# Kernel optimization log

Hardware: AMD Instinct MI355X
Metric: run time of the kernel (lower is better)

## Reference

```python
import jax, jax.numpy as jnp
import numpy as np

SLOPE = 0.01   # LeakyReLU default negative slope
EPS = 1e-5     # InstanceNorm eps
PAD = 6        # shift-search border

def _pad(x):
    # ReplicationPad (1,1) on H and W (depth pad is 0, depth==1 anyway)
    return jnp.pad(x, ((0, 0), (0, 0), (1, 1), (1, 1)), mode='edge')

def _conv(x, w, b):
    y = jax.lax.conv_general_dilated(x, w, (1, 1), 'VALID',
                                     dimension_numbers=('NCHW', 'OIHW', 'NCHW'))
    return y + b[None, :, None, None]

def _inorm(x):
    # InstanceNorm3d (affine=False) over (D,H,W); D==1 so over (H,W) per (b,c)
    m = jnp.mean(x, axis=(-2, -1), keepdims=True)
    v = jnp.mean((x - m) ** 2, axis=(-2, -1), keepdims=True)
    return (x - m) * jax.lax.rsqrt(v + EPS)

def _lrelu(x):
    return jnp.where(x >= 0, x, SLOPE * x)

def setup_inputs() -> dict:
    key = jax.random.key(0)
    ks = jax.random.split(key, 8)
    B, H, W = 8, 256, 256
    xIn = jax.random.normal(ks[0], (B, 1, H, W), jnp.float32)
    target = jax.random.normal(ks[1], (B, 1, H, W), jnp.float32)
    w0 = jax.random.normal(ks[2], (64, 1, 3, 3), jnp.float32) * 0.1
    b0 = jax.random.normal(ks[3], (64,), jnp.float32) * 0.1
    ws = jax.random.normal(ks[4], (7, 64, 64, 3, 3), jnp.float32) * 0.05
    bs = jax.random.normal(ks[5], (7, 64), jnp.float32) * 0.05
    wp = jax.random.normal(ks[6], (1, 64, 3, 3), jnp.float32) * 0.05
    bp = jax.random.normal(ks[7], (1,), jnp.float32) * 0.05
    return {'xIn': xIn, 'target': target, 'w0': w0, 'b0': b0,
            'ws': ws, 'bs': bs, 'wp': wp, 'bp': bp}

def reference(xIn, target, w0, b0, ws, bs, wp, bp):
    x = _lrelu(_inorm(_conv(_pad(xIn), w0, b0)))
    for i in range(7):
        x = _lrelu(_inorm(_conv(_pad(x), ws[i], bs[i])))
    # projection + residual
    hr = _conv(_pad(x), wp, bp) + xIn  # (B,1,H,W)

    # vectorized findBestLoss: 13x13 shift search
    B, C, H, W = hr.shape
    h, w = H - 2 * PAD, W - 2 * PAD
    t = hr.dtype.type(0) + target[..., PAD:H - PAD, PAD:W - PAD]  # (B,C,h,w)
    offs = jnp.stack(jnp.meshgrid(jnp.arange(13), jnp.arange(13),
                                  indexing='ij'), -1).reshape(-1, 2)  # (169,2)

    def _slice(off):
        return jax.lax.dynamic_slice(hr, (0, 0, off[0], off[1]), (B, C, h, w))

    crops = jax.vmap(_slice)(offs)  # (169,B,C,h,w)
    eq = jax.lax.stop_gradient(
        jnp.mean(t[None] - crops, axis=(2, 3, 4), keepdims=True))  # detached equalizer
    losses = jnp.mean((crops + eq - t[None]) ** 2, axis=(2, 3, 4))  # (169,B)
    loss = jnp.mean(jnp.min(losses, axis=0))
    return hr, loss
```

## Files before the change

### kernel.cpp

```cpp
#include <hip/hip_runtime.h>

#define B_ 8
#define C_ 64
#define HW_ 65536
#define SLOPE_ 0.01f
#define EPS_ 1e-5f
#define CROP_ 244
#define NPIX_ 59536.0f

typedef unsigned short u16;
typedef __attribute__((ext_vector_type(8))) _Float16 f16x8;
typedef __attribute__((ext_vector_type(2))) _Float16 f16x2;
typedef __attribute__((ext_vector_type(4))) float f32x4;

__device__ __forceinline__ int clampi(int v, int lo, int hi) { return v < lo ? lo : (v > hi ? hi : v); }

__device__ __forceinline__ u16 f2h(float f) {
    union { _Float16 h; u16 u; } v; v.h = (_Float16)f; return v.u;
}
__device__ __forceinline__ float h2f(u16 b) {
    union { u16 u; _Float16 h; } v; v.u = b; return (float)v.h;
}
__device__ __forceinline__ f16x2 lrelu2(f16x2 a) {
    const f16x2 z = {(_Float16)0.f, (_Float16)0.f};
    const f16x2 sl = {(_Float16)SLOPE_, (_Float16)SLOPE_};
    return __builtin_elementwise_max(a, z) + sl * __builtin_elementwise_min(a, z);
}

__global__ void wtrans_kernel(const float* __restrict__ ws, u16* __restrict__ wH) {
    int idx = blockIdx.x * 256 + threadIdx.x;
    if (idx >= 7 * 36864) return;
    int l = idx / 36864;
    int rem = idx - l * 36864;
    int frag = rem >> 9;
    int lj = rem & 511;
    int lane = lj >> 3, j = lj & 7;
    int tap = frag >> 3, kb = (frag >> 2) & 1, mt = frag & 3;
    int oc = (mt << 4) + (lane & 15);
    int ic = (kb << 5) + ((lane >> 4) << 3) + j;
    wH[idx] = f2h(ws[((l * 64 + oc) * 64 + ic) * 9 + tap]);
}

__global__ __launch_bounds__(256) void conv0_kernel(
    const float* __restrict__ xin, const float* __restrict__ w0,
    const float* __restrict__ b0, u16* __restrict__ yout) {
    __shared__ float w0s[576];
    __shared__ float b0s[64];
    int tid = threadIdx.x;
    for (int i = tid; i < 576; i += 256) w0s[i] = w0[i];
    if (tid < 64) b0s[tid] = b0[tid];
    __syncthreads();
    int b = blockIdx.x & 7;
    int px = (blockIdx.x >> 3) * 256 + tid;
    int pxg = (b << 16) + px;
    int y = px >> 8, x = px & 255;
    float xv[9];
#pragma unroll
    for (int ky = 0; ky < 3; ky++)
#pragma unroll
        for (int kx = 0; kx < 3; kx++)
            xv[ky * 3 + kx] = xin[(b << 16) + (clampi(y + ky - 1, 0, 255) << 8) + clampi(x + kx - 1, 0, 255)];
    float acc[64];
#pragma unroll
    for (int k = 0; k < 64; k++) acc[k] = b0s[k];
#pragma unroll
    for (int t = 0; t < 9; t++) {
        float v = xv[t];
#pragma unroll
        for (int k = 0; k < 64; k++) acc[k] = fmaf(v, w0s[k * 9 + t], acc[k]);
    }
    uint4* op = (uint4*)(yout + ((size_t)pxg << 6));
#pragma unroll
    for (int c8 = 0; c8 < 8; c8++) {
        uint4 o;
        o.x = (unsigned)f2h(acc[c8 * 8 + 0]) | ((unsigned)f2h(acc[c8 * 8 + 1]) << 16);
        o.y = (unsigned)f2h(acc[c8 * 8 + 2]) | ((unsigned)f2h(acc[c8 * 8 + 3]) << 16);
        o.z = (unsigned)f2h(acc[c8 * 8 + 4]) | ((unsigned)f2h(acc[c8 * 8 + 5]) << 16);
        o.w = (unsigned)f2h(acc[c8 * 8 + 6]) | ((unsigned)f2h(acc[c8 * 8 + 7]) << 16);
        op[c8] = o;
    }
}

__global__ __launch_bounds__(256) void stats0_kernel(const u16* __restrict__ yin, float* __restrict__ partial) {
    __shared__ float red[4][64][2];
    int tid = threadIdx.x;
    int b = blockIdx.x & 7, tile = blockIdx.x >> 3;
    int pxl = tid >> 3, c8 = tid & 7;
    float s[8], s2[8];
#pragma unroll
    for (int i = 0; i < 8; i++) { s[i] = 0.f; s2[i] = 0.f; }
    for (int it = 0; it < 8; it++) {
        int px = (tile << 8) + (it << 5) + pxl;
        f16x8 v = *(const f16x8*)(yin + ((((size_t)(b << 16)) + px) << 6) + (c8 << 3));
#pragma unroll
        for (int i = 0; i < 8; i++) {
            float f = (float)v[i];
            s[i] += f; s2[i] += f * f;
        }
    }
#pragma unroll
    for (int msk = 8; msk <= 32; msk <<= 1)
#pragma unroll
        for (int i = 0; i < 8; i++) {
            s[i] += __shfl_xor(s[i], msk);
            s2[i] += __shfl_xor(s2[i], msk);
        }
    int lane = tid & 63, wv = tid >> 6;
    if (lane < 8) {
#pragma unroll
        for (int i = 0; i < 8; i++) {
            red[wv][lane * 8 + i][0] = s[i];
            red[wv][lane * 8 + i][1] = s2[i];
        }
    }
    __syncthreads();
    if (tid < 128) {
        int oc = tid >> 1, k2 = tid & 1;
        float v = red[0][oc][k2] + red[1][oc][k2] + red[2][oc][k2] + red[3][oc][k2];
        partial[(((b << 8) + tile) << 7) + (oc << 1) + k2] = v;
    }
}

__global__ __launch_bounds__(64) void statfin_kernel(const float* __restrict__ partial, float* __restrict__ normp) {
    int b = blockIdx.x >> 6, oc = blockIdx.x & 63;
    int lane = threadIdx.x;
    float s = 0.f, s2 = 0.f;
#pragma unroll
    for (int i = 0; i < 4; i++) {
        int t = lane + (i << 6);
        const float* p = partial + (((b << 8) + t) << 7) + (oc << 1);
        s += p[0]; s2 += p[1];
    }
#pragma unroll
    for (int msk = 1; msk < 64; msk <<= 1) { s += __shfl_xor(s, msk); s2 += __shfl_xor(s2, msk); }
    if (lane == 0) {
        float mean = s * (1.0f / HW_);
        float var = s2 * (1.0f / HW_) - mean * mean;
        float inv = rsqrtf(var + EPS_);
        normp[blockIdx.x * 2] = inv;
        normp[blockIdx.x * 2 + 1] = -mean * inv;
    }
}

__global__ __launch_bounds__(256, 3) void conv_mid_kernel(
    const u16* __restrict__ yin, const float* __restrict__ normp,
    const u16* __restrict__ wH, const float* __restrict__ bias,
    u16* __restrict__ yout, float* __restrict__ partial) {
    __shared__ u16 s_in[324 * 64];
    __shared__ unsigned s_invk[32];
    __shared__ unsigned s_betak[32];
    __shared__ float s_bias[64];
    __shared__ float s_red[4][64][2];

    int tid = threadIdx.x;
    int b = blockIdx.x & 7;
    int tile = blockIdx.x >> 3;
    int ty = tile >> 4, tx = tile & 15;
    int y0 = ty << 4, x0 = tx << 4;

    if (tid < 64) s_bias[tid] = bias[tid];
    if (tid < 32) {
        float4 ld = ((const float4*)(normp + (b << 7)))[tid];
        union { unsigned u; f16x2 h; } iv, bv;
        iv.h = (f16x2){(_Float16)ld.x, (_Float16)ld.z};
        bv.h = (f16x2){(_Float16)ld.y, (_Float16)ld.w};
        s_invk[tid] = iv.u;
        s_betak[tid] = bv.u;
    }
    __syncthreads();

    for (int chunk = tid; chunk < 2592; chunk += 256) {
        int px = chunk >> 3, c8 = chunk & 7;
        int row = px / 18;
        int col = px - row * 18;
        int iy = clampi(y0 - 1 + row, 0, 255);
        int ix = clampi(x0 - 1 + col, 0, 255);
        union { uint4 q; f16x2 h2[4]; } ui, uo;
        ui.q = *(const uint4*)(yin + ((((size_t)(b << 16)) + (iy << 8) + ix) << 6) + (c8 << 3));
#pragma unroll
        for (int p = 0; p < 4; p++) {
            union { unsigned u; f16x2 h; } iv, bv;
            iv.u = s_invk[(c8 << 2) + p];
            bv.u = s_betak[(c8 << 2) + p];
            f16x2 a = ui.h2[p] * iv.h + bv.h;
            uo.h2[p] = lrelu2(a);
        }
        int phys = c8 ^ (px & 7);
        *(uint4*)(&s_in[(px << 6) + (phys << 3)]) = uo.q;
    }
    __syncthreads();

    int lane = tid & 63, wv = tid >> 6;
    int m = lane & 15, q = lane >> 4;
    int r0 = wv << 2;

    f32x4 acc[4][4];
#pragma unroll
    for (int a = 0; a < 4; a++)
#pragma unroll
        for (int c = 0; c < 4; c++) acc[a][c] = (f32x4){0.f, 0.f, 0.f, 0.f};

    const f16x8* wfp = (const f16x8*)wH;
    f16x8 wcur[8], wnxt[8];
#pragma unroll
    for (int f = 0; f < 8; f++) wcur[f] = wfp[(f << 6) + lane];

#pragma unroll 1
    for (int t = 0; t < 9; t++) {
        if (t < 8) {
            const f16x8* wn = wfp + ((t + 1) << 9);
#pragma unroll
            for (int f = 0; f < 8; f++) wnxt[f] = wn[(f << 6) + lane];
        }
        int ky = t / 3, kx = t - ky * 3;
#pragma unroll
        for (int nt = 0; nt < 4; nt++) {
            int row = r0 + nt + ky;
            int p = row * 18 + kx + m;
            int key = p & 7;
            const u16* pin = &s_in[p << 6];
            f16x8 bf0 = *(const f16x8*)(pin + ((q ^ key) << 3));
            f16x8 bf1 = *(const f16x8*)(pin + (((4 + q) ^ key) << 3));
#pragma unroll
            for (int mt = 0; mt < 4; mt++)
                acc[mt][nt] = __builtin_amdgcn_mfma_f32_16x16x32_f16(wcur[mt], bf0, acc[mt][nt], 0, 0, 0);
#pragma unroll
            for (int mt = 0; mt < 4; mt++)
                acc[mt][nt] = __builtin_amdgcn_mfma_f32_16x16x32_f16(wcur[4 + mt], bf1, acc[mt][nt], 0, 0, 0);
        }
        if (t < 8) {
#pragma unroll
            for (int f = 0; f < 8; f++) wcur[f] = wnxt[f];
        }
    }

    float ss[4][4], sq[4][4];
#pragma unroll
    for (int mt = 0; mt < 4; mt++)
#pragma unroll
        for (int r = 0; r < 4; r++) { ss[mt][r] = 0.f; sq[mt][r] = 0.f; }

#pragma unroll
    for (int mt = 0; mt < 4; mt++) {
        int ocb = (mt << 4) + (q << 2);
        float b0v = s_bias[ocb], b1v = s_bias[ocb + 1], b2v = s_bias[ocb + 2], b3v = s_bias[ocb + 3];
#pragma unroll
        for (int nt = 0; nt < 4; nt++) {
            f32x4 v = acc[mt][nt];
            float v0 = v.x + b0v, v1 = v.y + b1v, v2 = v.z + b2v, v3 = v.w + b3v;
            uint2 o;
            o.x = (unsigned)f2h(v0) | ((unsigned)f2h(v1) << 16);
            o.y = (unsigned)f2h(v2) | ((unsigned)f2h(v3) << 16);
            int y = y0 + r0 + nt, x = x0 + m;
            *(uint2*)(yout + ((((size_t)(b << 16)) + (y << 8) + x) << 6) + ocb) = o;
            ss[mt][0] += v0; ss[mt][1] += v1; ss[mt][2] += v2; ss[mt][3] += v3;
            sq[mt][0] += v0 * v0; sq[mt][1] += v1 * v1; sq[mt][2] += v2 * v2; sq[mt][3] += v3 * v3;
        }
    }
#pragma unroll
    for (int mt = 0; mt < 4; mt++)
#pragma unroll
        for (int r = 0; r < 4; r++) {
#pragma unroll
            for (int msk = 1; msk <= 8; msk <<= 1) {
                ss[mt][r] += __shfl_xor(ss[mt][r], msk);
                sq[mt][r] += __shfl_xor(sq[mt][r], msk);
            }
        }
    if (m == 0) {
#pragma unroll
        for (int mt = 0; mt < 4; mt++)
#pragma unroll
            for (int r = 0; r < 4; r++) {
                int oc = (mt << 4) + (q << 2) + r;
                s_red[wv][oc][0] = ss[mt][r];
                s_red[wv][oc][1] = sq[mt][r];
            }
    }
    __syncthreads();
    if (tid < 128) {
        int oc = tid >> 1, k2 = tid & 1;
        float v = s_red[0][oc][k2] + s_red[1][oc][k2] + s_red[2][oc][k2] + s_red[3][oc][k2];
        partial[(((b << 8) + tile) << 7) + (oc << 1) + k2] = v;
    }
}

__global__ __launch_bounds__(256) void proj_kernel(
    const u16* __restrict__ y7, const float* __restrict__ normp,
    const float* __restrict__ wp, const float* __restrict__ bp,
    const float* __restrict__ xin, float* __restrict__ out) {
    __shared__ u16 s_a[18 * 66 * 8];
    __shared__ unsigned s_invk[32];
    __shared__ unsigned s_betak[32];
    __shared__ unsigned s_w2[288];

    int tid = threadIdx.x;
    int b = blockIdx.x & 7, slab = blockIdx.x >> 3;
    int sy = slab >> 2, sx = slab & 3;
    int y0 = sy << 4, x0 = sx << 6;

    if (tid < 32) {
        float4 ld = ((const float4*)(normp + (b << 7)))[tid];
        union { unsigned u; f16x2 h; } iv, bv;
        iv.h = (f16x2){(_Float16)ld.x, (_Float16)ld.z};
        bv.h = (f16x2){(_Float16)ld.y, (_Float16)ld.w};
        s_invk[tid] = iv.u;
        s_betak[tid] = bv.u;
    }
    for (int i = tid; i < 288; i += 256) {
        int pr = i / 9, tap = i - pr * 9;
        int ch = pr << 1;
        s_w2[i] = (unsigned)f2h(wp[ch * 9 + tap]) | ((unsigned)f2h(wp[(ch + 1) * 9 + tap]) << 16);
    }
    __syncthreads();

    int col = tid & 63, prow = tid >> 6;
    float acc[4];
#pragma unroll
    for (int r = 0; r < 4; r++) acc[r] = bp[0];

    for (int c8 = 0; c8 < 8; c8++) {
        for (int idx = tid; idx < 1188; idx += 256) {
            int row = idx / 66;
            int cc = idx - row * 66;
            int iy = clampi(y0 - 1 + row, 0, 255);
            int ix = clampi(x0 - 1 + cc, 0, 255);
            union { uint4 q; f16x2 h2[4]; } ui, uo;
            ui.q = *(const uint4*)(y7 + ((((size_t)(b << 16)) + (iy << 8) + ix) << 6) + (c8 << 3));
#pragma unroll
            for (int p = 0; p < 4; p++) {
                union { unsigned u; f16x2 h; } iv, bv;
                iv.u = s_invk[(c8 << 2) + p];
                bv.u = s_betak[(c8 << 2) + p];
                uo.h2[p] = lrelu2(ui.h2[p] * iv.h + bv.h);
            }
            *(uint4*)(&s_a[idx << 3]) = uo.q;
        }
        __syncthreads();

#pragma unroll
        for (int ky = 0; ky < 3; ky++)
#pragma unroll
            for (int kx = 0; kx < 3; kx++) {
                int tap = ky * 3 + kx;
                float w[8];
#pragma unroll
                for (int p = 0; p < 4; p++) {
                    unsigned wu = s_w2[((c8 << 2) + p) * 9 + tap];
                    w[2 * p] = h2f((u16)(wu & 0xffff));
                    w[2 * p + 1] = h2f((u16)(wu >> 16));
                }
#pragma unroll
                for (int rr = 0; rr < 4; rr++) {
                    int lrow = prow * 4 + rr + ky;
                    f16x8 v = *(const f16x8*)(&s_a[(lrow * 66 + col + kx) << 3]);
#pragma unroll
                    for (int i = 0; i < 8; i++)
                        acc[rr] = fmaf((float)v[i], w[i], acc[rr]);
                }
            }
        __syncthreads();
    }

#pragma unroll
    for (int rr = 0; rr < 4; rr++) {
        int pxg = (b << 16) + ((y0 + prow * 4 + rr) << 8) + x0 + col;
        out[pxg] = acc[rr] + xin[pxg];
    }
}

__global__ __launch_bounds__(256) void loss_main_kernel(
    const float* __restrict__ hr, const float* __restrict__ target,
    float* __restrict__ lossS) {
    int b = blockIdx.x & 7, off = blockIdx.x >> 3;
    int oy = off / 13, ox = off - oy * 13;
    const float* hp = hr + b * HW_ + (oy << 8) + ox;
    const float* tp = target + b * HW_ + (6 << 8) + 6;
    float s = 0.f, s2 = 0.f;
    for (int i = threadIdx.x; i < CROP_ * CROP_; i += 256) {
        int y = i / CROP_;
        int x = i - y * CROP_;
        float d = hp[(y << 8) + x] - tp[(y << 8) + x];
        s += d; s2 += d * d;
    }
    __shared__ float rs[4], rs2[4];
#pragma unroll
    for (int msk = 1; msk < 64; msk <<= 1) { s += __shfl_xor(s, msk); s2 += __shfl_xor(s2, msk); }
    int lane = threadIdx.x & 63, wv = threadIdx.x >> 6;
    if (lane == 0) { rs[wv] = s; rs2[wv] = s2; }
    __syncthreads();
    if (threadIdx.x == 0) {
        lossS[(off * 8 + b) * 2] = rs[0] + rs[1] + rs[2] + rs[3];
        lossS[(off * 8 + b) * 2 + 1] = rs2[0] + rs2[1] + rs2[2] + rs2[3];
    }
}

__global__ void loss_final_kernel(const float* __restrict__ lossS, float* __restrict__ out) {
    int b = threadIdx.x;
    float mn = 0.f;
    if (b < 8) {
        mn = 1e30f;
        for (int off = 0; off < 169; off++) {
            float s = lossS[(off * 8 + b) * 2];
            float s2 = lossS[(off * 8 + b) * 2 + 1];
            float m = s * (1.0f / NPIX_);
            float L = s2 * (1.0f / NPIX_) - m * m;
            mn = fminf(mn, L);
        }
    }
#pragma unroll
    for (int msk = 1; msk < 8; msk <<= 1) mn += __shfl_xor(mn, msk);
    if (b == 0) out[0] = mn * 0.125f;
}

extern "C" void kernel_launch(void* const* d_in, const int* in_sizes, int n_in,
                              void* d_out, int out_size, void* d_ws, size_t ws_size,
                              hipStream_t stream) {
    const float* xIn    = (const float*)d_in[0];
    const float* target = (const float*)d_in[1];
    const float* w0     = (const float*)d_in[2];
    const float* b0     = (const float*)d_in[3];
    const float* wsAll  = (const float*)d_in[4];
    const float* bsAll  = (const float*)d_in[5];
    const float* wp     = (const float*)d_in[6];
    const float* bp     = (const float*)d_in[7];
    float* out = (float*)d_out;

    float* normp   = (float*)d_ws;
    float* partial = normp + 1024;
    float* lossS   = partial + 262144;
    u16*  wH       = (u16*)(lossS + 2704);
    u16*  bufA     = wH + 258048;
    u16*  bufB     = bufA + 33554432;

    wtrans_kernel<<<1008, 256, 0, stream>>>(wsAll, wH);
    conv0_kernel<<<2048, 256, 0, stream>>>(xIn, w0, b0, bufA);
    stats0_kernel<<<2048, 256, 0, stream>>>(bufA, partial);
    statfin_kernel<<<512, 64, 0, stream>>>(partial, normp);
    for (int l = 0; l < 7; l++) {
        const u16* in = (l & 1) ? bufB : bufA;
        u16* o = (l & 1) ? bufA : bufB;
        conv_mid_kernel<<<2048, 256, 0, stream>>>(
            in, normp, wH + l * 36864, bsAll + l * 64, o, partial);
        statfin_kernel<<<512, 64, 0, stream>>>(partial, normp);
    }
    proj_kernel<<<512, 256, 0, stream>>>(bufB, normp, wp, bp, xIn, out);
    loss_main_kernel<<<1352, 256, 0, stream>>>(out, target, lossS);
    loss_final_kernel<<<1, 64, 0, stream>>>(lossS, out + 524288);
}
```

Before: 763.1 us.

## Enlarge conv tiles to 32x16 and restructure shift-search loss with row strips

The mid conv kernel now computes 32x16 output tiles per block, with 8 row-tiles per wave. This halves halo overhead and gives more reuse of each loaded weight fragment, at the cost of larger LDS use, lower occupancy (launch bound 2) and dropping the weight prefetch double-buffer. The loss computation is restructured so each block loads 4 rows of hr and target into shared memory and accumulates all 13 horizontal shifts at once. This replaces 169 separate strided full-image passes and adds an intermediate reduction kernel.

New measurement: 730.0 us. 4.3% less time.

```diff
diff --git a/kernel.cpp b/kernel.cpp
--- a/kernel.cpp
+++ b/kernel.cpp
@@ -121,14 +121,12 @@
     }
 }
 
-__global__ __launch_bounds__(64) void statfin_kernel(const float* __restrict__ partial, float* __restrict__ normp) {
+__global__ __launch_bounds__(64) void statfin_kernel(const float* __restrict__ partial, float* __restrict__ normp, int ntiles) {
     int b = blockIdx.x >> 6, oc = blockIdx.x & 63;
     int lane = threadIdx.x;
     float s = 0.f, s2 = 0.f;
-#pragma unroll
-    for (int i = 0; i < 4; i++) {
-        int t = lane + (i << 6);
-        const float* p = partial + (((b << 8) + t) << 7) + (oc << 1);
+    for (int t = lane; t < ntiles; t += 64) {
+        const float* p = partial + (((size_t)(b * ntiles + t)) << 7) + (oc << 1);
         s += p[0]; s2 += p[1];
     }
 #pragma unroll
@@ -142,21 +140,21 @@
     }
 }
 
-__global__ __launch_bounds__(256, 3) void conv_mid_kernel(
+__global__ __launch_bounds__(256, 2) void conv_mid_kernel(
     const u16* __restrict__ yin, const float* __restrict__ normp,
     const u16* __restrict__ wH, const float* __restrict__ bias,
     u16* __restrict__ yout, float* __restrict__ partial) {
-    __shared__ u16 s_in[324 * 64];
+    __shared__ u16 s_in[612 * 64];
     __shared__ unsigned s_invk[32];
     __shared__ unsigned s_betak[32];
     __shared__ float s_bias[64];
-    __shared__ float s_red[4][64][2];
+    float* s_red = (float*)s_in;
 
     int tid = threadIdx.x;
     int b = blockIdx.x & 7;
     int tile = blockIdx.x >> 3;
     int ty = tile >> 4, tx = tile & 15;
-    int y0 = ty << 4, x0 = tx << 4;
+    int y0 = ty << 5, x0 = tx << 4;
 
     if (tid < 64) s_bias[tid] = bias[tid];
     if (tid < 32) {
@@ -169,7 +167,7 @@
     }
     __syncthreads();
 
-    for (int chunk = tid; chunk < 2592; chunk += 256) {
+    for (int chunk = tid; chunk < 4896; chunk += 256) {
         int px = chunk >> 3, c8 = chunk & 7;
         int row = px / 18;
         int col = px - row * 18;
@@ -182,8 +180,7 @@
             union { unsigned u; f16x2 h; } iv, bv;
             iv.u = s_invk[(c8 << 2) + p];
             bv.u = s_betak[(c8 << 2) + p];
-            f16x2 a = ui.h2[p] * iv.h + bv.h;
-            uo.h2[p] = lrelu2(a);
+            uo.h2[p] = lrelu2(ui.h2[p] * iv.h + bv.h);
         }
         int phys = c8 ^ (px & 7);
         *(uint4*)(&s_in[(px << 6) + (phys << 3)]) = uo.q;
@@ -192,47 +189,38 @@
 
     int lane = tid & 63, wv = tid >> 6;
     int m = lane & 15, q = lane >> 4;
-    int r0 = wv << 2;
-
-    f32x4 acc[4][4];
+    int r0 = wv << 3;
+
+    f32x4 acc[4][8];
 #pragma unroll
     for (int a = 0; a < 4; a++)
 #pragma unroll
-        for (int c = 0; c < 4; c++) acc[a][c] = (f32x4){0.f, 0.f, 0.f, 0.f};
+        for (int c = 0; c < 8; c++) acc[a][c] = (f32x4){0.f, 0.f, 0.f, 0.f};
 
     const f16x8* wfp = (const f16x8*)wH;
-    f16x8 wcur[8], wnxt[8];
-#pragma unroll
-    for (int f = 0; f < 8; f++) wcur[f] = wfp[(f << 6) + lane];
-
 #pragma unroll 1
     for (int t = 0; t < 9; t++) {
-        if (t < 8) {
-            const f16x8* wn = wfp + ((t + 1) << 9);
-#pragma unroll
-            for (int f = 0; f < 8; f++) wnxt[f] = wn[(f << 6) + lane];
-        }
         int ky = t / 3, kx = t - ky * 3;
-#pragma unroll
-        for (int nt = 0; nt < 4; nt++) {
-            int row = r0 + nt + ky;
-            int p = row * 18 + kx + m;
+        const f16x8* wn = wfp + (t << 9);
+        f16x8 wf[8];
+#pragma unroll
+        for (int f = 0; f < 8; f++) wf[f] = wn[(f << 6) + lane];
+#pragma unroll
+        for (int nt = 0; nt < 8; nt++) {
+            int p = (r0 + nt + ky) * 18 + kx + m;
             int key = p & 7;
             const u16* pin = &s_in[p << 6];
             f16x8 bf0 = *(const f16x8*)(pin + ((q ^ key) << 3));
             f16x8 bf1 = *(const f16x8*)(pin + (((4 + q) ^ key) << 3));
 #pragma unroll
             for (int mt = 0; mt < 4; mt++)
-                acc[mt][nt] = __builtin_amdgcn_mfma_f32_16x16x32_f16(wcur[mt], bf0, acc[mt][nt], 0, 0, 0);
+                acc[mt][nt] = __builtin_amdgcn_mfma_f32_16x16x32_f16(wf[mt], bf0, acc[mt][nt], 0, 0, 0);
 #pragma unroll
             for (int mt = 0; mt < 4; mt++)
-                acc[mt][nt] = __builtin_amdgcn_mfma_f32_16x16x32_f16(wcur[4 + mt], bf1, acc[mt][nt], 0, 0, 0);
-        }
-        if (t < 8) {
-#pragma unroll
-            for (int f = 0; f < 8; f++) wcur[f] = wnxt[f];
-        }
-    }
+                acc[mt][nt] = __builtin_amdgcn_mfma_f32_16x16x32_f16(wf[4 + mt], bf1, acc[mt][nt], 0, 0, 0);
+        }
+    }
+    __syncthreads();
 
     float ss[4][4], sq[4][4];
 #pragma unroll
@@ -245,7 +233,7 @@
         int ocb = (mt << 4) + (q << 2);
         float b0v = s_bias[ocb], b1v = s_bias[ocb + 1], b2v = s_bias[ocb + 2], b3v = s_bias[ocb + 3];
 #pragma unroll
-        for (int nt = 0; nt < 4; nt++) {
+        for (int nt = 0; nt < 8; nt++) {
             f32x4 v = acc[mt][nt];
             float v0 = v.x + b0v, v1 = v.y + b1v, v2 = v.z + b2v, v3 = v.w + b3v;
             uint2 o;
@@ -273,15 +261,16 @@
 #pragma unroll
             for (int r = 0; r < 4; r++) {
                 int oc = (mt << 4) + (q << 2) + r;
-                s_red[wv][oc][0] = ss[mt][r];
-                s_red[wv][oc][1] = sq[mt][r];
+                s_red[(wv * 64 + oc) * 2] = ss[mt][r];
+                s_red[(wv * 64 + oc) * 2 + 1] = sq[mt][r];
             }
     }
     __syncthreads();
     if (tid < 128) {
         int oc = tid >> 1, k2 = tid & 1;
-        float v = s_red[0][oc][k2] + s_red[1][oc][k2] + s_red[2][oc][k2] + s_red[3][oc][k2];
-        partial[(((b << 8) + tile) << 7) + (oc << 1) + k2] = v;
+        float v = s_red[(0 * 64 + oc) * 2 + k2] + s_red[(1 * 64 + oc) * 2 + k2]
+                + s_red[(2 * 64 + oc) * 2 + k2] + s_red[(3 * 64 + oc) * 2 + k2];
+        partial[(((b << 7) + tile) << 7) + (oc << 1) + k2] = v;
     }
 }
 
@@ -369,44 +358,88 @@
     }
 }
 
-__global__ __launch_bounds__(256) void loss_main_kernel(
+__global__ __launch_bounds__(256) void loss_strip_kernel(
     const float* __restrict__ hr, const float* __restrict__ target,
-    float* __restrict__ lossS) {
+    float* __restrict__ partial2) {
+    __shared__ float s_hr[4][256];
+    __shared__ float s_t[4][244];
+    __shared__ float s_r2[4][13][2];
+
+    int tid = threadIdx.x;
+    int b = blockIdx.x & 7;
+    int rest = blockIdx.x >> 3;
+    int oy = rest % 13;
+    int strip = rest / 13;
+    int y0 = strip << 2;
+
+    for (int i = tid; i < 1024; i += 256) {
+        int r = i >> 8, x = i & 255;
+        s_hr[r][x] = hr[(b << 16) + ((y0 + oy + r) << 8) + x];
+    }
+    for (int i = tid; i < 976; i += 256) {
+        int r = i / 244, x = i - r * 244;
+        s_t[r][x] = target[(b << 16) + ((y0 + r + 6) << 8) + 6 + x];
+    }
+    __syncthreads();
+
+    float s[13], s2[13];
+#pragma unroll
+    for (int o = 0; o < 13; o++) { s[o] = 0.f; s2[o] = 0.f; }
+    if (tid < 244) {
+#pragma unroll
+        for (int r = 0; r < 4; r++) {
+            float tv = s_t[r][tid];
+#pragma unroll
+            for (int o = 0; o < 13; o++) {
+                float d = s_hr[r][tid + o] - tv;
+                s[o] += d; s2[o] += d * d;
+            }
+        }
+    }
+#pragma unroll
+    for (int msk = 1; msk < 64; msk <<= 1)
+#pragma unroll
+        for (int o = 0; o < 13; o++) {
+            s[o] += __shfl_xor(s[o], msk);
+            s2[o] += __shfl_xor(s2[o], msk);
+        }
+    int lane = tid & 63, wv = tid >> 6;
+    if (lane == 0) {
+#pragma unroll
+        for (int o = 0; o < 13; o++) { s_r2[wv][o][0] = s[o]; s_r2[wv][o][1] = s2[o]; }
+    }
+    __syncthreads();
+    if (tid < 26) {
+        int o = tid >> 1, k = tid & 1;
+        float v = s_r2[0][o][k] + s_r2[1][o][k] + s_r2[2][o][k] + s_r2[3][o][k];
+        int off = oy * 13 + o;
+        partial2[(((b * 61 + strip) * 169) + off) * 2 + k] = v;
+    }
+}
+
+__global__ __launch_bounds__(64) void loss_mid_kernel(
+    const float* __restrict__ partial2, float* __restrict__ lossM) {
     int b = blockIdx.x & 7, off = blockIdx.x >> 3;
-    int oy = off / 13, ox = off - oy * 13;
-    const float* hp = hr + b * HW_ + (oy << 8) + ox;
-    const float* tp = target + b * HW_ + (6 << 8) + 6;
+    int lane = threadIdx.x;
     float s = 0.f, s2 = 0.f;
-    for (int i = threadIdx.x; i < CROP_ * CROP_; i += 256) {
-        int y = i / CROP_;
-        int x = i - y * CROP_;
-        float d = hp[(y << 8) + x] - tp[(y << 8) + x];
-        s += d; s2 += d * d;
-    }
-    __shared__ float rs[4], rs2[4];
+    if (lane < 61) {
+        const float* p = partial2 + (((b * 61 + lane) * 169) + off) * 2;
+        s = p[0]; s2 = p[1];
+    }
 #pragma unroll
     for (int msk = 1; msk < 64; msk <<= 1) { s += __shfl_xor(s, msk); s2 += __shfl_xor(s2, msk); }
-    int lane = threadIdx.x & 63, wv = threadIdx.x >> 6;
-    if (lane == 0) { rs[wv] = s; rs2[wv] = s2; }
-    __syncthreads();
-    if (threadIdx.x == 0) {
-        lossS[(off * 8 + b) * 2] = rs[0] + rs[1] + rs[2] + rs[3];
-        lossS[(off * 8 + b) * 2 + 1] = rs2[0] + rs2[1] + rs2[2] + rs2[3];
-    }
-}
-
-__global__ void loss_final_kernel(const float* __restrict__ lossS, float* __restrict__ out) {
+    if (lane == 0) {
+        float m = s * (1.0f / NPIX_);
+        lossM[off * 8 + b] = s2 * (1.0f / NPIX_) - m * m;
+    }
+}
+
+__global__ void loss_final_kernel(const float* __restrict__ lossM, float* __restrict__ out) {
     int b = threadIdx.x;
     float mn = 0.f;
     if (b < 8) {
         mn = 1e30f;
-        for (int off = 0; off < 169; off++) {
-            float s = lossS[(off * 8 + b) * 2];
-            float s2 = lossS[(off * 8 + b) * 2 + 1];
-            float m = s * (1.0f / NPIX_);
-            float L = s2 * (1.0f / NPIX_) - m * m;
-            mn = fminf(mn, L);
-        }
+        for (int off = 0; off < 169; off++) mn = fminf(mn, lossM[off * 8 + b]);
     }
 #pragma unroll
     for (int msk = 1; msk < 8; msk <<= 1) mn += __shfl_xor(mn, msk);
@@ -426,25 +459,27 @@
     const float* bp     = (const float*)d_in[7];
     float* out = (float*)d_out;
 
-    float* normp   = (float*)d_ws;
-    float* partial = normp + 1024;
-    float* lossS   = partial + 262144;
-    u16*  wH       = (u16*)(lossS + 2704);
-    u16*  bufA     = wH + 258048;
-    u16*  bufB     = bufA + 33554432;
+    float* normp    = (float*)d_ws;
+    float* partial  = normp + 1024;
+    float* partial2 = partial + 262144;
+    float* lossM    = partial2 + 164944;
+    u16*  wH        = (u16*)(lossM + 1352);
+    u16*  bufA      = wH + 258048;
+    u16*  bufB      = bufA + 33554432;
 
     wtrans_kernel<<<1008, 256, 0, stream>>>(wsAll, wH);
     conv0_kernel<<<2048, 256, 0, stream>>>(xIn, w0, b0, bufA);
     stats0_kernel<<<2048, 256, 0, stream>>>(bufA, partial);
-    statfin_kernel<<<512, 64, 0, stream>>>(partial, normp);
+    statfin_kernel<<<512, 64, 0, stream>>>(partial, normp, 256);
     for (int l = 0; l < 7; l++) {
         const u16* in = (l & 1) ? bufB : bufA;
         u16* o = (l & 1) ? bufA : bufB;
-        conv_mid_kernel<<<2048, 256, 0, stream>>>(
+        conv_mid_kernel<<<1024, 256, 0, stream>>>(
             in, normp, wH + l * 36864, bsAll + l * 64, o, partial);
-        statfin_kernel<<<512, 64, 0, stream>>>(partial, normp);
+        statfin_kernel<<<512, 64, 0, stream>>>(partial, normp, 128);
     }
     proj_kernel<<<512, 256, 0, stream>>>(bufB, normp, wp, bp, xIn, out);
-    loss_main_kernel<<<1352, 256, 0, stream>>>(out, target, lossS);
-    loss_final_kernel<<<1, 64, 0, stream>>>(lossS, out + 524288);
-}
+    loss_strip_kernel<<<6344, 256, 0, stream>>>(out, target, partial2);
+    loss_mid_kernel<<<1352, 64, 0, stream>>>(partial2, lossM);
+    loss_final_kernel<<<1, 64, 0, stream>>>(lossM, out + 524288);
+}
```
